# Kernel optimization log

Hardware: AMD Instinct MI355X
Metric: run time of the kernel (lower is better)

## Reference

```python
import jax, jax.numpy as jnp
import numpy as np

N_NODES = 50000
N_EDGES = 800000
DIM = 64


def gat_layer(h, d, src, dst, V, W, U, A, n):
    # t = fcV(d): [E, 1]
    t = d @ V.T
    # z = fcW(h), z_i = fcU(h): [N, out]
    z = h @ W.T
    z_i = h @ U.T
    out_dim = z.shape[1]
    # attn_fc(concat([z_src, z_dst, t])) decomposed to avoid materializing concat
    a_src, a_dst, a_e = A[:out_dim], A[out_dim:2 * out_dim], A[2 * out_dim:]
    e = z[src] @ a_src + z[dst] @ a_dst + t @ a_e  # [E]
    e = jax.nn.leaky_relu(e, negative_slope=0.01)
    # segment (per-destination) softmax over incoming edges
    m = jax.ops.segment_max(e, dst, num_segments=n)
    ex = jnp.exp(e - m[dst])
    denom = jax.ops.segment_sum(ex, dst, num_segments=n)
    alpha = ex / denom[dst]  # [E]
    # weighted scatter-sum aggregation of neighbor z
    agg = jax.ops.segment_sum(alpha[:, None] * z[src], dst, num_segments=n)
    deg = jax.ops.segment_sum(jnp.ones_like(e), dst, num_segments=n)
    # DGL leaves zero in-degree nodes at 0 (reduce_func never called)
    return jnp.where((deg > 0)[:, None], jax.nn.relu(z_i + agg), 0.0)


def setup_inputs() -> dict:
    key = jax.random.key(0)
    ks = jax.random.split(key, 12)
    s = 0.1
    return {
        "h": jax.random.normal(ks[0], (N_NODES, DIM), dtype=jnp.float32),
        "d": jax.random.normal(ks[1], (N_EDGES, 1), dtype=jnp.float32),
        "src": jax.random.randint(ks[2], (N_EDGES,), 0, N_NODES, dtype=jnp.int32),
        "dst": jax.random.randint(ks[3], (N_EDGES,), 0, N_NODES, dtype=jnp.int32),
        "V0": jax.random.normal(ks[4], (1, 1), dtype=jnp.float32) * s,
        "W0": jax.random.normal(ks[5], (DIM, DIM), dtype=jnp.float32) * s,
        "U0": jax.random.normal(ks[6], (DIM, DIM), dtype=jnp.float32) * s,
        "A0": jax.random.normal(ks[7], (2 * DIM + 1,), dtype=jnp.float32) * s,
        "V1": jax.random.normal(ks[8], (1, 1), dtype=jnp.float32) * s,
        "W1": jax.random.normal(ks[9], (DIM, DIM), dtype=jnp.float32) * s,
        "U1": jax.random.normal(ks[10], (DIM, DIM), dtype=jnp.float32) * s,
        "A1": jax.random.normal(ks[11], (2 * DIM + 1,), dtype=jnp.float32) * s,
    }


def reference(h, d, src, dst, V0, W0, U0, A0, V1, W1, U1, A1):
    n = h.shape[0]
    h1 = gat_layer(h, d, src, dst, V0, W0, U0, A0, n)
    h2 = gat_layer(h1, d, src, dst, V1, W1, U1, A1, n)
    return h2
```

## Files before the change

### kernel.cpp

```cpp
#include <hip/hip_runtime.h>
#include <math.h>

#define N_NODES 50000
#define N_EDGES 800000
#define DIM 64
#define NPB 128
#define NPB_SHIFT 7
#define NBUCKET 391
#define CAP 2560
#define EPB 2048
#define NBLK 391
#define NB_NL 782
#define NB_GAT 3125

__device__ __forceinline__ ushort f2bf(float x) {
    unsigned b = __float_as_uint(x);
    return (ushort)((b + 0x7FFFu + ((b >> 16) & 1u)) >> 16);
}
__device__ __forceinline__ float bf2f(ushort u) {
    return __uint_as_float(((unsigned)u) << 16);
}

template<bool IN_BF16>
__device__ __forceinline__ void nl_body(
    int vb, const void* __restrict__ hin, const float* __restrict__ W,
    const float* __restrict__ U, const float* __restrict__ A,
    ushort* __restrict__ zb, ushort* __restrict__ zib,
    float* __restrict__ s_src, float* __restrict__ s_dst,
    float (*Ws)[DIM + 1], float (*Us)[DIM + 1], float (*hs)[DIM + 1])
{
    const int tid = threadIdx.x;
    const int row0 = vb * 64;

    for (int i = tid; i < 1024; i += 256) {
        int r = i >> 4, c = (i & 15) * 4;
        float4 w4 = ((const float4*)W)[i];
        float4 u4 = ((const float4*)U)[i];
        Ws[r][c] = w4.x; Ws[r][c + 1] = w4.y; Ws[r][c + 2] = w4.z; Ws[r][c + 3] = w4.w;
        Us[r][c] = u4.x; Us[r][c + 1] = u4.y; Us[r][c + 2] = u4.z; Us[r][c + 3] = u4.w;
        int n = row0 + r;
        float4 h4 = make_float4(0.f, 0.f, 0.f, 0.f);
        if (n < N_NODES) {
            if (IN_BF16) {
                ushort4 hb = ((const ushort4*)hin)[((size_t)n * DIM + c) >> 2];
                h4 = make_float4(bf2f(hb.x), bf2f(hb.y), bf2f(hb.z), bf2f(hb.w));
            } else {
                h4 = ((const float4*)hin)[((size_t)n * DIM + c) >> 2];
            }
        }
        hs[r][c] = h4.x; hs[r][c + 1] = h4.y; hs[r][c + 2] = h4.z; hs[r][c + 3] = h4.w;
    }
    __syncthreads();

    const int rb = (tid >> 4) * 4;
    const int cb = (tid & 15) * 4;

    float accz[4][4] = {{0}}, accu[4][4] = {{0}};
    #pragma unroll 8
    for (int k = 0; k < DIM; ++k) {
        float hv[4], wv[4], uv[4];
        #pragma unroll
        for (int r = 0; r < 4; ++r) hv[r] = hs[rb + r][k];
        #pragma unroll
        for (int c = 0; c < 4; ++c) { wv[c] = Ws[cb + c][k]; uv[c] = Us[cb + c][k]; }
        #pragma unroll
        for (int r = 0; r < 4; ++r)
            #pragma unroll
            for (int c = 0; c < 4; ++c) {
                accz[r][c] += hv[r] * wv[c];
                accu[r][c] += hv[r] * uv[c];
            }
    }

    float asrc[4], adst[4];
    #pragma unroll
    for (int c = 0; c < 4; ++c) { asrc[c] = A[cb + c]; adst[c] = A[DIM + cb + c]; }

    float ps[4], pd[4];
    #pragma unroll
    for (int r = 0; r < 4; ++r) {
        int n = row0 + rb + r;
        if (n < N_NODES) {
            ushort4 vz, vu;
            vz.x = f2bf(accz[r][0]); vz.y = f2bf(accz[r][1]);
            vz.z = f2bf(accz[r][2]); vz.w = f2bf(accz[r][3]);
            vu.x = f2bf(accu[r][0]); vu.y = f2bf(accu[r][1]);
            vu.z = f2bf(accu[r][2]); vu.w = f2bf(accu[r][3]);
            *(ushort4*)&zb[(size_t)n * DIM + cb]  = vz;
            *(ushort4*)&zib[(size_t)n * DIM + cb] = vu;
        }
        float s = 0.f, t = 0.f;
        #pragma unroll
        for (int c = 0; c < 4; ++c) { s += accz[r][c] * asrc[c]; t += accz[r][c] * adst[c]; }
        ps[r] = s; pd[r] = t;
    }
    #pragma unroll
    for (int m = 1; m < 16; m <<= 1) {
        #pragma unroll
        for (int r = 0; r < 4; ++r) {
            ps[r] += __shfl_xor(ps[r], m, 64);
            pd[r] += __shfl_xor(pd[r], m, 64);
        }
    }
    if ((tid & 15) == 0) {
        #pragma unroll
        for (int r = 0; r < 4; ++r) {
            int n = row0 + rb + r;
            if (n < N_NODES) { s_src[n] = ps[r]; s_dst[n] = pd[r]; }
        }
    }
}

__device__ __forceinline__ void partition_body(
    int vb, const int* __restrict__ src, const int* __restrict__ dst,
    const float* __restrict__ dfeat, int* __restrict__ gcursor,
    int2* __restrict__ part, int* __restrict__ h)
{
    for (int b = threadIdx.x; b < NBUCKET; b += 256) h[b] = 0;
    __syncthreads();
    int base = vb * EPB;
    #pragma unroll
    for (int j = 0; j < EPB / 256; ++j) {
        int e = base + j * 256 + threadIdx.x;
        if (e < N_EDGES) atomicAdd(&h[dst[e] >> NPB_SHIFT], 1);
    }
    __syncthreads();
    for (int b = threadIdx.x; b < NBUCKET; b += 256) {
        int v = h[b];
        h[b] = v ? (b * CAP + atomicAdd(&gcursor[b], v)) : 0;
    }
    __syncthreads();
    #pragma unroll
    for (int j = 0; j < EPB / 256; ++j) {
        int e = base + j * 256 + threadIdx.x;
        if (e < N_EDGES) {
            int d = dst[e];
            int pos = atomicAdd(&h[d >> NPB_SHIFT], 1);
            part[pos] = make_int2(((d & (NPB - 1)) << 16) | src[e], __float_as_int(dfeat[e]));
        }
    }
}

struct K1NL { float Ws[DIM][DIM + 1]; float Us[DIM][DIM + 1]; float hs[64][DIM + 1]; };
union K1U { K1NL nl; int hist[NBUCKET]; };

__global__ __launch_bounds__(256) void k1_nl_part(
    const float* __restrict__ h, const float* __restrict__ W0,
    const float* __restrict__ U0, const float* __restrict__ A0,
    ushort* __restrict__ zb, ushort* __restrict__ zib,
    float* __restrict__ ssrc, float* __restrict__ sdst,
    const int* __restrict__ src, const int* __restrict__ dst,
    const float* __restrict__ dd, int* __restrict__ gcursor, int2* __restrict__ part)
{
    __shared__ K1U sm;
    int bid = blockIdx.x;
    int m = bid % 3;
    if (m == 2)
        partition_body(bid / 3, src, dst, dd, gcursor, part, sm.hist);
    else
        nl_body<false>((bid / 3) * 2 + m, h, W0, U0, A0, zb, zib, ssrc, sdst,
                       sm.nl.Ws, sm.nl.Us, sm.nl.hs);
}

__global__ __launch_bounds__(256) void node_linear2(
    const ushort* __restrict__ h1b, const float* __restrict__ W,
    const float* __restrict__ U, const float* __restrict__ A,
    ushort* __restrict__ zb, ushort* __restrict__ zib,
    float* __restrict__ ssrc, float* __restrict__ sdst)
{
    __shared__ K1NL sm;
    nl_body<true>(blockIdx.x, h1b, W, U, A, zb, zib, ssrc, sdst, sm.Ws, sm.Us, sm.hs);
}

__global__ __launch_bounds__(256) void bucket_sort(
    const int2* __restrict__ part, const int* __restrict__ gcursor,
    unsigned* __restrict__ edata, int2* __restrict__ rowse)
{
    __shared__ int cnt[NPB];
    __shared__ int cur[NPB];
    int b = blockIdx.x, t = threadIdx.x;
    int beg = b * CAP, end = beg + gcursor[b];
    if (t < NPB) cnt[t] = 0;
    __syncthreads();
    for (int i = beg + t; i < end; i += 256) atomicAdd(&cnt[part[i].x >> 16], 1);
    __syncthreads();
    if (t < NPB) cur[t] = cnt[t];
    __syncthreads();
    for (int off = 1; off < NPB; off <<= 1) {
        int a = (t < NPB && t >= off) ? cur[t - off] : 0;
        __syncthreads();
        if (t < NPB) cur[t] += a;
        __syncthreads();
    }
    if (t < NPB) {
        int n = (b << NPB_SHIFT) + t;
        int cv = cnt[t];
        int st = beg + cur[t] - cv;
        if (n < N_NODES) rowse[n] = make_int2(st, st + cv);
        cur[t] = st;
    }
    __syncthreads();
    for (int i = beg + t; i < end; i += 256) {
        int2 ed = part[i];
        int loc = ed.x >> 16;
        int pos = atomicAdd(&cur[loc], 1);
        edata[pos] = ((unsigned)(ed.x & 0xFFFF) << 16) | (unsigned)f2bf(__int_as_float(ed.y));
    }
}

template<bool OUT_BF16>
__global__ __launch_bounds__(256) void gat_fused(
    const int2* __restrict__ rowse, const unsigned* __restrict__ edata,
    const float* __restrict__ s_src, const float* __restrict__ s_dst,
    const ushort* __restrict__ zb, const ushort* __restrict__ zib,
    const float* __restrict__ V, const float* __restrict__ A,
    void* __restrict__ out)
{
    const int n = blockIdx.x * 16 + (threadIdx.x >> 4);
    const int q = threadIdx.x & 15;
    const int gbase = threadIdx.x & 48;

    int2 se = rowse[n];
    int beg = se.x, end = se.y;
    if (beg == end) {
        if (OUT_BF16) {
            ushort4 zz; zz.x = zz.y = zz.z = zz.w = 0;
            ((ushort4*)out)[(size_t)n * 16 + q] = zz;
        } else {
            ((float4*)out)[(size_t)n * 16 + q] = make_float4(0.f, 0.f, 0.f, 0.f);
        }
        return;
    }

    float vae = V[0] * A[2 * DIM];
    float sd = s_dst[n];

    float l = 0.f;
    float4 a0 = make_float4(0.f, 0.f, 0.f, 0.f);
    float4 a1 = make_float4(0.f, 0.f, 0.f, 0.f);

    for (int c0 = beg; c0 < end; c0 += 16) {
        int c = c0 + q;
        bool valid = c < end;
        unsigned w = valid ? edata[c] : 0u;
        int s = (int)(w >> 16);
        float dv = bf2f((ushort)(w & 0xFFFFu));
        float e = s_src[s] + sd + dv * vae;
        e = (e >= 0.f) ? e : 0.01f * e;
        float ex = valid ? __expf(e) : 0.f;

        float cs = ex;
        #pragma unroll
        for (int off = 8; off >= 1; off >>= 1) cs += __shfl_xor(cs, off, 16);
        l += cs;

        unsigned w2 = valid ? (((unsigned)s << 16) | (unsigned)f2bf(ex)) : 0u;

        int cnt = min(16, end - c0);
        for (int k = 0; k < cnt; k += 8) {
            unsigned wsj[8];
            ushort4 v[8];
            #pragma unroll
            for (int j = 0; j < 8; ++j) {
                wsj[j] = __shfl(w2, gbase + k + j, 64);
                v[j] = *(const ushort4*)&zb[((size_t)(wsj[j] >> 16) << 6) + (q << 2)];
            }
            #pragma unroll
            for (int j = 0; j < 8; ++j) {
                float ej = bf2f((ushort)(wsj[j] & 0xFFFFu));
                if (j & 1) {
                    a1.x += ej * bf2f(v[j].x); a1.y += ej * bf2f(v[j].y);
                    a1.z += ej * bf2f(v[j].z); a1.w += ej * bf2f(v[j].w);
                } else {
                    a0.x += ej * bf2f(v[j].x); a0.y += ej * bf2f(v[j].y);
                    a0.z += ej * bf2f(v[j].z); a0.w += ej * bf2f(v[j].w);
                }
            }
        }
    }
    float inv = 1.f / l;
    ushort4 zu = ((const ushort4*)zib)[(size_t)n * 16 + q];
    float4 o;
    o.x = fmaxf(bf2f(zu.x) + (a0.x + a1.x) * inv, 0.f);
    o.y = fmaxf(bf2f(zu.y) + (a0.y + a1.y) * inv, 0.f);
    o.z = fmaxf(bf2f(zu.z) + (a0.z + a1.z) * inv, 0.f);
    o.w = fmaxf(bf2f(zu.w) + (a0.w + a1.w) * inv, 0.f);
    if (OUT_BF16) {
        ushort4 ob;
        ob.x = f2bf(o.x); ob.y = f2bf(o.y); ob.z = f2bf(o.z); ob.w = f2bf(o.w);
        ((ushort4*)out)[(size_t)n * 16 + q] = ob;
    } else {
        ((float4*)out)[(size_t)n * 16 + q] = o;
    }
}

extern "C" void kernel_launch(void* const* d_in, const int* in_sizes, int n_in,
                              void* d_out, int out_size, void* d_ws, size_t ws_size,
                              hipStream_t stream)
{
    const float* h  = (const float*)d_in[0];
    const float* dd = (const float*)d_in[1];
    const int* src  = (const int*)d_in[2];
    const int* dst  = (const int*)d_in[3];
    const float* V0 = (const float*)d_in[4];
    const float* W0 = (const float*)d_in[5];
    const float* U0 = (const float*)d_in[6];
    const float* A0 = (const float*)d_in[7];
    const float* V1 = (const float*)d_in[8];
    const float* W1 = (const float*)d_in[9];
    const float* U1 = (const float*)d_in[10];
    const float* A1 = (const float*)d_in[11];

    const size_t ND = (size_t)N_NODES * DIM;
    float* ws    = (float*)d_ws;
    ushort* zb   = (ushort*)ws;
    ushort* zib  = zb + ND;
    ushort* h1b  = zib + ND;
    float* ssrc  = ws + (3 * ND) / 2;
    float* sdst  = ssrc + N_NODES;
    int2*  rowse = (int2*)(sdst + N_NODES);
    int2*  part  = rowse + N_NODES;
    unsigned* edata = (unsigned*)(part + (size_t)NBUCKET * CAP);
    int*   gcursor  = (int*)(edata + (size_t)NBUCKET * CAP);
    float* out   = (float*)d_out;

    hipMemsetAsync(gcursor, 0, NBUCKET * sizeof(int), stream);
    k1_nl_part<<<3 * NBLK, 256, 0, stream>>>(h, W0, U0, A0, zb, zib, ssrc, sdst,
                                             src, dst, dd, gcursor, part);
    bucket_sort<<<NBUCKET, 256, 0, stream>>>(part, gcursor, edata, rowse);
    gat_fused<true><<<NB_GAT, 256, 0, stream>>>(rowse, edata, ssrc, sdst, zb, zib, V0, A0, h1b);
    node_linear2<<<NB_NL, 256, 0, stream>>>(h1b, W1, U1, A1, zb, zib, ssrc, sdst);
    gat_fused<false><<<NB_GAT, 256, 0, stream>>>(rowse, edata, ssrc, sdst, zb, zib, V1, A1, out);
}
```

Measured before the change: 195.1 us.

## Fuse bucket sort, layer-1 GAT aggregation and layer-2 node linear into one kernel

```diff
diff --git a/kernel.cpp b/kernel.cpp
--- a/kernel.cpp
+++ b/kernel.cpp
@@ -12,6 +12,7 @@
 #define NBLK 391
 #define NB_NL 782
 #define NB_GAT 3125
+#define BPAD 6
 
 __device__ __forceinline__ ushort f2bf(float x) {
     unsigned b = __float_as_uint(x);
@@ -21,9 +22,8 @@
     return __uint_as_float(((unsigned)u) << 16);
 }
 
-template<bool IN_BF16>
-__device__ __forceinline__ void nl_body(
-    int vb, const void* __restrict__ hin, const float* __restrict__ W,
+__device__ __forceinline__ void nl_body1(
+    int vb, const float* __restrict__ hin, const float* __restrict__ W,
     const float* __restrict__ U, const float* __restrict__ A,
     ushort* __restrict__ zb, ushort* __restrict__ zib,
     float* __restrict__ s_src, float* __restrict__ s_dst,
@@ -40,14 +40,7 @@
         Us[r][c] = u4.x; Us[r][c + 1] = u4.y; Us[r][c + 2] = u4.z; Us[r][c + 3] = u4.w;
         int n = row0 + r;
         float4 h4 = make_float4(0.f, 0.f, 0.f, 0.f);
-        if (n < N_NODES) {
-            if (IN_BF16) {
-                ushort4 hb = ((const ushort4*)hin)[((size_t)n * DIM + c) >> 2];
-                h4 = make_float4(bf2f(hb.x), bf2f(hb.y), bf2f(hb.z), bf2f(hb.w));
-            } else {
-                h4 = ((const float4*)hin)[((size_t)n * DIM + c) >> 2];
-            }
-        }
+        if (n < N_NODES) h4 = ((const float4*)hin)[((size_t)n * DIM + c) >> 2];
         hs[r][c] = h4.x; hs[r][c + 1] = h4.y; hs[r][c + 2] = h4.z; hs[r][c + 3] = h4.w;
     }
     __syncthreads();
@@ -158,63 +151,222 @@
     if (m == 2)
         partition_body(bid / 3, src, dst, dd, gcursor, part, sm.hist);
     else
-        nl_body<false>((bid / 3) * 2 + m, h, W0, U0, A0, zb, zib, ssrc, sdst,
-                       sm.nl.Ws, sm.nl.Us, sm.nl.hs);
-}
-
-__global__ __launch_bounds__(256) void node_linear2(
-    const ushort* __restrict__ h1b, const float* __restrict__ W,
-    const float* __restrict__ U, const float* __restrict__ A,
-    ushort* __restrict__ zb, ushort* __restrict__ zib,
-    float* __restrict__ ssrc, float* __restrict__ sdst)
-{
-    __shared__ K1NL sm;
-    nl_body<true>(blockIdx.x, h1b, W, U, A, zb, zib, ssrc, sdst, sm.Ws, sm.Us, sm.hs);
-}
-
-__global__ __launch_bounds__(256) void bucket_sort(
+        nl_body1((bid / 3) * 2 + m, h, W0, U0, A0, zb, zib, ssrc, sdst,
+                 sm.nl.Ws, sm.nl.Us, sm.nl.hs);
+}
+
+struct K2Srt { int cnt[NPB]; int cur[NPB]; unsigned esh[CAP]; };
+struct K2WU  { ushort Ws[DIM][DIM + BPAD]; ushort Us[DIM][DIM + BPAD]; };
+union K2U { K2Srt srt; K2WU wu; };
+
+__global__ __launch_bounds__(256) void k2_sort_gat_nl(
     const int2* __restrict__ part, const int* __restrict__ gcursor,
-    unsigned* __restrict__ edata, int2* __restrict__ rowse)
-{
-    __shared__ int cnt[NPB];
-    __shared__ int cur[NPB];
-    int b = blockIdx.x, t = threadIdx.x;
-    int beg = b * CAP, end = beg + gcursor[b];
-    if (t < NPB) cnt[t] = 0;
-    __syncthreads();
-    for (int i = beg + t; i < end; i += 256) atomicAdd(&cnt[part[i].x >> 16], 1);
-    __syncthreads();
-    if (t < NPB) cur[t] = cnt[t];
+    unsigned* __restrict__ edata, int2* __restrict__ rowse,
+    const float* __restrict__ ssrc1, const float* __restrict__ sdst1,
+    const ushort* __restrict__ zb1, const ushort* __restrict__ zib1,
+    const float* __restrict__ V0, const float* __restrict__ A0,
+    const float* __restrict__ W1, const float* __restrict__ U1, const float* __restrict__ A1,
+    ushort* __restrict__ zb2, ushort* __restrict__ zib2,
+    float* __restrict__ ssrc2, float* __restrict__ sdst2)
+{
+    __shared__ K2U u;
+    __shared__ ushort h1t[NPB][DIM + BPAD];
+
+    const int b = blockIdx.x, t = threadIdx.x;
+    const int n0 = b << NPB_SHIFT;
+    const int beg = b * CAP;
+    const int cntE = gcursor[b];
+    const int end = beg + cntE;
+
+    if (t < NPB) u.srt.cnt[t] = 0;
+    __syncthreads();
+    for (int i = beg + t; i < end; i += 256) atomicAdd(&u.srt.cnt[part[i].x >> 16], 1);
+    __syncthreads();
+    int cv = 0;
+    if (t < NPB) { cv = u.srt.cnt[t]; u.srt.cur[t] = cv; }
     __syncthreads();
     for (int off = 1; off < NPB; off <<= 1) {
-        int a = (t < NPB && t >= off) ? cur[t - off] : 0;
+        int a = (t < NPB && t >= off) ? u.srt.cur[t - off] : 0;
         __syncthreads();
-        if (t < NPB) cur[t] += a;
+        if (t < NPB) u.srt.cur[t] += a;
         __syncthreads();
     }
     if (t < NPB) {
-        int n = (b << NPB_SHIFT) + t;
-        int cv = cnt[t];
-        int st = beg + cur[t] - cv;
-        if (n < N_NODES) rowse[n] = make_int2(st, st + cv);
-        cur[t] = st;
+        int n = n0 + t;
+        int stl = u.srt.cur[t] - cv;
+        if (n < N_NODES) rowse[n] = make_int2(beg + stl, beg + stl + cv);
+        u.srt.cur[t] = stl;
     }
     __syncthreads();
     for (int i = beg + t; i < end; i += 256) {
         int2 ed = part[i];
         int loc = ed.x >> 16;
-        int pos = atomicAdd(&cur[loc], 1);
-        edata[pos] = ((unsigned)(ed.x & 0xFFFF) << 16) | (unsigned)f2bf(__int_as_float(ed.y));
-    }
-}
-
-template<bool OUT_BF16>
-__global__ __launch_bounds__(256) void gat_fused(
+        int pos = atomicAdd(&u.srt.cur[loc], 1);
+        unsigned pk = ((unsigned)(ed.x & 0xFFFF) << 16) | (unsigned)f2bf(__int_as_float(ed.y));
+        u.srt.esh[pos] = pk;
+        edata[beg + pos] = pk;
+    }
+    __syncthreads();
+
+    {
+        const float vae = V0[0] * A0[2 * DIM];
+        const int gid = t >> 4, q = t & 15, gbase = t & 48;
+        for (int p = 0; p < 8; ++p) {
+            int tn = p * 16 + gid;
+            int n = n0 + tn;
+            if (n >= N_NODES) continue;
+            int endl = u.srt.cur[tn];
+            int stl  = endl - u.srt.cnt[tn];
+            if (stl == endl) {
+                ushort4 zz; zz.x = zz.y = zz.z = zz.w = 0;
+                *(ushort4*)&h1t[tn][q << 2] = zz;
+                continue;
+            }
+            float sd = sdst1[n];
+            float l = 0.f;
+            float4 a0v = make_float4(0.f, 0.f, 0.f, 0.f);
+            float4 a1v = make_float4(0.f, 0.f, 0.f, 0.f);
+            for (int c0 = stl; c0 < endl; c0 += 16) {
+                int c = c0 + q;
+                bool valid = c < endl;
+                unsigned w = valid ? u.srt.esh[c] : 0u;
+                int s = (int)(w >> 16);
+                float dv = bf2f((ushort)(w & 0xFFFFu));
+                float e = ssrc1[s] + sd + dv * vae;
+                e = (e >= 0.f) ? e : 0.01f * e;
+                float ex = valid ? __expf(e) : 0.f;
+
+                float cs = ex;
+                #pragma unroll
+                for (int off = 8; off >= 1; off >>= 1) cs += __shfl_xor(cs, off, 16);
+                l += cs;
+
+                unsigned w2 = valid ? (((unsigned)s << 16) | (unsigned)f2bf(ex)) : 0u;
+                int cnt = min(16, endl - c0);
+                for (int k = 0; k < cnt; k += 8) {
+                    unsigned wsj[8];
+                    ushort4 v[8];
+                    #pragma unroll
+                    for (int j = 0; j < 8; ++j) {
+                        wsj[j] = __shfl(w2, gbase + k + j, 64);
+                        v[j] = *(const ushort4*)&zb1[((size_t)(wsj[j] >> 16) << 6) + (q << 2)];
+                    }
+                    #pragma unroll
+                    for (int j = 0; j < 8; ++j) {
+                        float ej = bf2f((ushort)(wsj[j] & 0xFFFFu));
+                        if (j & 1) {
+                            a1v.x += ej * bf2f(v[j].x); a1v.y += ej * bf2f(v[j].y);
+                            a1v.z += ej * bf2f(v[j].z); a1v.w += ej * bf2f(v[j].w);
+                        } else {
+                            a0v.x += ej * bf2f(v[j].x); a0v.y += ej * bf2f(v[j].y);
+                            a0v.z += ej * bf2f(v[j].z); a0v.w += ej * bf2f(v[j].w);
+                        }
+                    }
+                }
+            }
+            float inv = 1.f / l;
+            ushort4 zu = *(const ushort4*)&zib1[((size_t)n << 6) + (q << 2)];
+            ushort4 ob;
+            ob.x = f2bf(fmaxf(bf2f(zu.x) + (a0v.x + a1v.x) * inv, 0.f));
+            ob.y = f2bf(fmaxf(bf2f(zu.y) + (a0v.y + a1v.y) * inv, 0.f));
+            ob.z = f2bf(fmaxf(bf2f(zu.z) + (a0v.z + a1v.z) * inv, 0.f));
+            ob.w = f2bf(fmaxf(bf2f(zu.w) + (a0v.w + a1v.w) * inv, 0.f));
+            *(ushort4*)&h1t[tn][q << 2] = ob;
+        }
+    }
+    __syncthreads();
+
+    for (int i = t; i < 1024; i += 256) {
+        int r = i >> 4, c = (i & 15) * 4;
+        float4 w4 = ((const float4*)W1)[i];
+        float4 u4 = ((const float4*)U1)[i];
+        ushort4 wp, up;
+        wp.x = f2bf(w4.x); wp.y = f2bf(w4.y); wp.z = f2bf(w4.z); wp.w = f2bf(w4.w);
+        up.x = f2bf(u4.x); up.y = f2bf(u4.y); up.z = f2bf(u4.z); up.w = f2bf(u4.w);
+        *(ushort4*)&u.wu.Ws[r][c] = wp;
+        *(ushort4*)&u.wu.Us[r][c] = up;
+    }
+    __syncthreads();
+
+    const int rb = (t >> 4) * 4;
+    const int cb = (t & 15) * 4;
+    float asrc[4], adst[4];
+    #pragma unroll
+    for (int c = 0; c < 4; ++c) { asrc[c] = A1[cb + c]; adst[c] = A1[DIM + cb + c]; }
+
+    for (int half = 0; half < 2; ++half) {
+        const int rowb = half * 64;
+        float accz[4][4] = {{0}}, accu[4][4] = {{0}};
+        #pragma unroll 4
+        for (int k = 0; k < DIM; k += 4) {
+            float hv[4][4], wv[4][4], uv[4][4];
+            #pragma unroll
+            for (int r = 0; r < 4; ++r) {
+                ushort4 hb = *(const ushort4*)&h1t[rowb + rb + r][k];
+                hv[r][0] = bf2f(hb.x); hv[r][1] = bf2f(hb.y);
+                hv[r][2] = bf2f(hb.z); hv[r][3] = bf2f(hb.w);
+            }
+            #pragma unroll
+            for (int c = 0; c < 4; ++c) {
+                ushort4 wb = *(const ushort4*)&u.wu.Ws[cb + c][k];
+                ushort4 ub = *(const ushort4*)&u.wu.Us[cb + c][k];
+                wv[c][0] = bf2f(wb.x); wv[c][1] = bf2f(wb.y);
+                wv[c][2] = bf2f(wb.z); wv[c][3] = bf2f(wb.w);
+                uv[c][0] = bf2f(ub.x); uv[c][1] = bf2f(ub.y);
+                uv[c][2] = bf2f(ub.z); uv[c][3] = bf2f(ub.w);
+            }
+            #pragma unroll
+            for (int r = 0; r < 4; ++r)
+                #pragma unroll
+                for (int c = 0; c < 4; ++c) {
+                    accz[r][c] += hv[r][0] * wv[c][0] + hv[r][1] * wv[c][1]
+                                + hv[r][2] * wv[c][2] + hv[r][3] * wv[c][3];
+                    accu[r][c] += hv[r][0] * uv[c][0] + hv[r][1] * uv[c][1]
+                                + hv[r][2] * uv[c][2] + hv[r][3] * uv[c][3];
+                }
+        }
+        float ps[4], pd[4];
+        #pragma unroll
+        for (int r = 0; r < 4; ++r) {
+            int n = n0 + rowb + rb + r;
+            if (n < N_NODES) {
+                ushort4 vz, vu;
+                vz.x = f2bf(accz[r][0]); vz.y = f2bf(accz[r][1]);
+                vz.z = f2bf(accz[r][2]); vz.w = f2bf(accz[r][3]);
+                vu.x = f2bf(accu[r][0]); vu.y = f2bf(accu[r][1]);
+                vu.z = f2bf(accu[r][2]); vu.w = f2bf(accu[r][3]);
+                *(ushort4*)&zb2[(size_t)n * DIM + cb]  = vz;
+                *(ushort4*)&zib2[(size_t)n * DIM + cb] = vu;
+            }
+            float s = 0.f, tt = 0.f;
+            #pragma unroll
+            for (int c = 0; c < 4; ++c) { s += accz[r][c] * asrc[c]; tt += accz[r][c] * adst[c]; }
+            ps[r] = s; pd[r] = tt;
+        }
+        #pragma unroll
+        for (int m = 1; m < 16; m <<= 1) {
+            #pragma unroll
+            for (int r = 0; r < 4; ++r) {
+                ps[r] += __shfl_xor(ps[r], m, 64);
+                pd[r] += __shfl_xor(pd[r], m, 64);
+            }
+        }
+        if ((t & 15) == 0) {
+            #pragma unroll
+            for (int r = 0; r < 4; ++r) {
+                int n = n0 + rowb + rb + r;
+                if (n < N_NODES) { ssrc2[n] = ps[r]; sdst2[n] = pd[r]; }
+            }
+        }
+    }
+}
+
+__global__ __launch_bounds__(256) void gat_fused2(
     const int2* __restrict__ rowse, const unsigned* __restrict__ edata,
     const float* __restrict__ s_src, const float* __restrict__ s_dst,
     const ushort* __restrict__ zb, const ushort* __restrict__ zib,
     const float* __restrict__ V, const float* __restrict__ A,
-    void* __restrict__ out)
+    float* __restrict__ out)
 {
     const int n = blockIdx.x * 16 + (threadIdx.x >> 4);
     const int q = threadIdx.x & 15;
@@ -223,12 +375,7 @@
     int2 se = rowse[n];
     int beg = se.x, end = se.y;
     if (beg == end) {
-        if (OUT_BF16) {
-            ushort4 zz; zz.x = zz.y = zz.z = zz.w = 0;
-            ((ushort4*)out)[(size_t)n * 16 + q] = zz;
-        } else {
-            ((float4*)out)[(size_t)n * 16 + q] = make_float4(0.f, 0.f, 0.f, 0.f);
-        }
+        ((float4*)out)[(size_t)n * 16 + q] = make_float4(0.f, 0.f, 0.f, 0.f);
         return;
     }
 
@@ -285,13 +432,7 @@
     o.y = fmaxf(bf2f(zu.y) + (a0.y + a1.y) * inv, 0.f);
     o.z = fmaxf(bf2f(zu.z) + (a0.z + a1.z) * inv, 0.f);
     o.w = fmaxf(bf2f(zu.w) + (a0.w + a1.w) * inv, 0.f);
-    if (OUT_BF16) {
-        ushort4 ob;
-        ob.x = f2bf(o.x); ob.y = f2bf(o.y); ob.z = f2bf(o.z); ob.w = f2bf(o.w);
-        ((ushort4*)out)[(size_t)n * 16 + q] = ob;
-    } else {
-        ((float4*)out)[(size_t)n * 16 + q] = o;
-    }
+    ((float4*)out)[(size_t)n * 16 + q] = o;
 }
 
 extern "C" void kernel_launch(void* const* d_in, const int* in_sizes, int n_in,
@@ -313,22 +454,25 @@
 
     const size_t ND = (size_t)N_NODES * DIM;
     float* ws    = (float*)d_ws;
-    ushort* zb   = (ushort*)ws;
-    ushort* zib  = zb + ND;
-    ushort* h1b  = zib + ND;
-    float* ssrc  = ws + (3 * ND) / 2;
-    float* sdst  = ssrc + N_NODES;
-    int2*  rowse = (int2*)(sdst + N_NODES);
+    ushort* zb1  = (ushort*)ws;
+    ushort* zib1 = zb1 + ND;
+    ushort* zb2  = zib1 + ND;
+    ushort* zib2 = zb2 + ND;
+    float* ssrc1 = ws + 2 * ND;
+    float* sdst1 = ssrc1 + N_NODES;
+    float* ssrc2 = sdst1 + N_NODES;
+    float* sdst2 = ssrc2 + N_NODES;
+    int2*  rowse = (int2*)(sdst2 + N_NODES);
     int2*  part  = rowse + N_NODES;
     unsigned* edata = (unsigned*)(part + (size_t)NBUCKET * CAP);
     int*   gcursor  = (int*)(edata + (size_t)NBUCKET * CAP);
     float* out   = (float*)d_out;
 
     hipMemsetAsync(gcursor, 0, NBUCKET * sizeof(int), stream);
-    k1_nl_part<<<3 * NBLK, 256, 0, stream>>>(h, W0, U0, A0, zb, zib, ssrc, sdst,
+    k1_nl_part<<<3 * NBLK, 256, 0, stream>>>(h, W0, U0, A0, zb1, zib1, ssrc1, sdst1,
                                              src, dst, dd, gcursor, part);
-    bucket_sort<<<NBUCKET, 256, 0, stream>>>(part, gcursor, edata, rowse);
-    gat_fused<true><<<NB_GAT, 256, 0, stream>>>(rowse, edata, ssrc, sdst, zb, zib, V0, A0, h1b);
-    node_linear2<<<NB_NL, 256, 0, stream>>>(h1b, W1, U1, A1, zb, zib, ssrc, sdst);
-    gat_fused<false><<<NB_GAT, 256, 0, stream>>>(rowse, edata, ssrc, sdst, zb, zib, V1, A1, out);
-}
+    k2_sort_gat_nl<<<NBUCKET, 256, 0, stream>>>(part, gcursor, edata, rowse,
+                                                ssrc1, sdst1, zb1, zib1, V0, A0,
+                                                W1, U1, A1, zb2, zib2, ssrc2, sdst2);
+    gat_fused2<<<NB_GAT, 256, 0, stream>>>(rowse, edata, ssrc2, sdst2, zb2, zib2, V1, A1, out);
+}
```

Result: no change. 193.7 us (-0.7%).
